# Optimization experiments

Measured on AMD Instinct MI355X. Metric: run time of the kernel, lower is better.

Reference implementation:

```python
import jax, jax.numpy as jnp
import numpy as np

N = 50000      # nodes
E = 800000     # edges (before self loops)
F_IN = 64
H = 128
OUT = 1
G = 512        # graphs in batch
NEG_SLOPE = 0.2


def setup_inputs() -> dict:
    key = jax.random.key(0)
    ks = jax.random.split(key, 16)
    s_in = 1.0 / np.sqrt(F_IN)
    s_h = 1.0 / np.sqrt(H)
    return {
        "x": jax.random.normal(ks[0], (N, F_IN), jnp.float32),
        "edge_index": jax.random.randint(ks[1], (2, E), 0, N, jnp.int64),
        "edge_weight": jax.random.uniform(ks[2], (E,), jnp.float32),
        "batch": jnp.sort(jax.random.randint(ks[3], (N,), 0, G, jnp.int64)),
        # GATv2 layer 1 (lin_l, lin_r, att, bias)
        "Wl1": jax.random.normal(ks[4], (F_IN, H), jnp.float32) * s_in,
        "bl1": jnp.zeros((H,), jnp.float32),
        "Wr1": jax.random.normal(ks[5], (F_IN, H), jnp.float32) * s_in,
        "br1": jnp.zeros((H,), jnp.float32),
        "att1": jax.random.normal(ks[6], (H,), jnp.float32) * s_h,
        "b1": jnp.zeros((H,), jnp.float32),
        # GATv2 layer 2
        "Wl2": jax.random.normal(ks[7], (H, H), jnp.float32) * s_h,
        "bl2": jnp.zeros((H,), jnp.float32),
        "Wr2": jax.random.normal(ks[8], (H, H), jnp.float32) * s_h,
        "br2": jnp.zeros((H,), jnp.float32),
        "att2": jax.random.normal(ks[9], (H,), jnp.float32) * s_h,
        "b2": jnp.zeros((H,), jnp.float32),
        # final linear head
        "Wlin": jax.random.normal(ks[10], (H, OUT), jnp.float32) * s_h,
        "blin": jnp.zeros((OUT,), jnp.float32),
    }


def gatv2_conv(x, src, dst, Wl, bl, Wr, br, att, bias):
    """PyG GATv2Conv, heads=1: alpha = softmax_dst(att . leaky_relu(xl[src]+xr[dst]));
    out[dst] = sum alpha * xl[src] + bias. Self loops already in (src, dst)."""
    xl = x @ Wl + bl                       # [N,H]  source transform
    xr = x @ Wr + br                       # [N,H]  destination transform
    e = xl[src] + xr[dst]                  # [Etot,H]
    logits = jax.nn.leaky_relu(e, NEG_SLOPE) @ att   # [Etot]
    # segment softmax over destination nodes (self loops -> every node nonempty)
    m = jax.ops.segment_max(logits, dst, num_segments=N)
    ea = jnp.exp(logits - m[dst])
    denom = jax.ops.segment_sum(ea, dst, num_segments=N)
    alpha = ea / denom[dst]
    out = jax.ops.segment_sum(alpha[:, None] * xl[src], dst, num_segments=N)
    return out + bias


def reference(x, edge_index, edge_weight, batch,
              Wl1, bl1, Wr1, br1, att1, b1,
              Wl2, bl2, Wr2, br2, att2, b2,
              Wlin, blin):
    # add self loops (GATv2Conv default add_self_loops=True); edge_weight unused by GATv2
    loops = jnp.arange(N, dtype=edge_index.dtype)
    src = jnp.concatenate([edge_index[0], loops])
    dst = jnp.concatenate([edge_index[1], loops])

    h = jax.nn.relu(gatv2_conv(x, src, dst, Wl1, bl1, Wr1, br1, att1, b1))
    h = jax.nn.relu(gatv2_conv(h, src, dst, Wl2, bl2, Wr2, br2, att2, b2))

    # global mean pool over graphs
    sums = jax.ops.segment_sum(h, batch, num_segments=G)          # [G,H]
    cnt = jax.ops.segment_sum(jnp.ones((N,), h.dtype), batch, num_segments=G)
    pooled = sums / jnp.maximum(cnt, 1.0)[:, None]

    return pooled @ Wlin + blin                                   # [G,OUT]
```

## Files before the change

### kernel.cpp

```cpp
#include <hip/hip_runtime.h>
#include <hip/hip_fp16.h>
#include <math.h>

#define N_NODES 50000
#define N_EDGES 800000
#define F_IN    64
#define H_DIM   128
#define N_GRAPH 512
#define NEG_SLOPE 0.2f

typedef __attribute__((ext_vector_type(8))) short short8;
typedef __attribute__((ext_vector_type(4))) float f32x4;
typedef __attribute__((ext_vector_type(2))) float f32x2;

#define NBIN   196
#define NBLK1  391
#define NBB    (NBIN * NBLK1)
#define SCANA_NB ((NBB + 255) / 256)

__device__ __forceinline__ void bsplit(float v, unsigned short& h, unsigned short& l) {
    unsigned u = __float_as_uint(v);
    h = (unsigned short)(u >> 16);
    float hf = __uint_as_float(u & 0xFFFF0000u);
    float r = v - hf;
    l = (unsigned short)(__float_as_uint(r) >> 16);
}
__device__ __forceinline__ float bjoin(unsigned short h, unsigned short l) {
    return __uint_as_float(((unsigned)h) << 16) + __uint_as_float(((unsigned)l) << 16);
}

#define NB_PX 3125
#define NB_PW 192
__global__ __launch_bounds__(256) void k_prep(
    const float* __restrict__ x,
    const float* __restrict__ Wl1, const float* __restrict__ Wr1,
    const float* __restrict__ Wl2, const float* __restrict__ Wr2,
    const int* __restrict__ dst,
    unsigned short* __restrict__ Xhi, unsigned short* __restrict__ Xlo,
    unsigned short* __restrict__ WThi, unsigned short* __restrict__ WTlo,
    int* __restrict__ lrank, int* __restrict__ bcnt)
{
    __shared__ int cnt_lds[NBIN];
    const int bid = blockIdx.x, tid = threadIdx.x;
    if (bid < NB_PX) {
        int i4 = (bid * 256 + tid) * 4;
        if (i4 < N_NODES * F_IN) {
            float4 v = *(const float4*)(x + i4);
            ushort4 h, l;
            bsplit(v.x, h.x, l.x); bsplit(v.y, h.y, l.y);
            bsplit(v.z, h.z, l.z); bsplit(v.w, h.w, l.w);
            *(ushort4*)(Xhi + i4) = h;
            *(ushort4*)(Xlo + i4) = l;
        }
    } else if (bid < NB_PX + NB_PW) {
        int idx = (bid - NB_PX) * 256 + tid;
        if (idx < 49152) {
            const float* W; int K, li, base, o;
            if (idx < 8192)       { W = Wl1; K = 64;  li = idx;         base = 0;     o = 0; }
            else if (idx < 16384) { W = Wr1; K = 64;  li = idx - 8192;  base = 0;     o = 1; }
            else if (idx < 32768) { W = Wl2; K = 128; li = idx - 16384; base = 16384; o = 0; }
            else                  { W = Wr2; K = 128; li = idx - 32768; base = 16384; o = 1; }
            int c = li / K, k = li - c * K;
            int g = c >> 4, n16 = c & 15;
            int kkblk = k >> 5, quad = (k >> 3) & 3, j = k & 7;
            int off = base + kkblk * 8192 + o * 4096 + g * 512 + (quad * 16 + n16) * 8 + j;
            unsigned short h, l;
            bsplit(W[k * 128 + c], h, l);
            WThi[off] = h; WTlo[off] = l;
        }
    } else {
        const int b2 = bid - NB_PX - NB_PW;
        if (tid < NBIN) cnt_lds[tid] = 0;
        __syncthreads();
#pragma unroll
        for (int it = 0; it < 8; ++it) {
            int e = b2 * 2048 + it * 256 + tid;
            if (e < N_EDGES) {
                int d = dst[e];
                lrank[e] = atomicAdd(&cnt_lds[d >> 8], 1);
            }
        }
        __syncthreads();
        if (tid < NBIN) bcnt[tid * NBLK1 + b2] = cnt_lds[tid];
    }
}

__global__ __launch_bounds__(256) void k_scanA(const int* __restrict__ bcnt,
                                               int* __restrict__ bbase,
                                               int* __restrict__ partials) {
    __shared__ int s[256];
    int t = threadIdx.x, gid = blockIdx.x * 256 + t;
    int v = (gid < NBB) ? bcnt[gid] : 0;
    s[t] = v;
    __syncthreads();
    for (int off = 1; off < 256; off <<= 1) {
        int x = (t >= off) ? s[t - off] : 0;
        __syncthreads();
        s[t] += x;
        __syncthreads();
    }
    if (gid < NBB) bbase[gid] = s[t] - v;
    if (t == 255) partials[blockIdx.x] = s[t];
}

__global__ __launch_bounds__(256) void k_scanB(int* __restrict__ bbase,
                                               const int* __restrict__ partials) {
    __shared__ int red[256];
    const int t = threadIdx.x, b = blockIdx.x;
    int acc = 0;
    for (int j = t; j < b; j += 256) acc += partials[j];
    red[t] = acc;
    __syncthreads();
    for (int off = 128; off > 0; off >>= 1) {
        if (t < off) red[t] += red[t + off];
        __syncthreads();
    }
    int base = red[0];
    int gid = b * 256 + t;
    if (gid < NBB) bbase[gid] += base;
}

__global__ __launch_bounds__(256) void k_bin2(const int* __restrict__ src,
                                              const int* __restrict__ dst,
                                              const int* __restrict__ lrank,
                                              const int* __restrict__ bbase,
                                              unsigned* __restrict__ ebin) {
    int e = blockIdx.x * 256 + threadIdx.x;
    if (e < N_EDGES) {
        int d = dst[e];
        int pos = bbase[(d >> 8) * NBLK1 + (e >> 11)] + lrank[e];
        ebin[pos] = (unsigned)src[e] | ((unsigned)(d & 255) << 16);
    }
}

__global__ __launch_bounds__(256) void k_bin3(const unsigned* __restrict__ ebin,
                                              const int* __restrict__ bbase,
                                              int* __restrict__ offsets,
                                              int* __restrict__ col_src) {
    __shared__ int cnt2[256];
    __shared__ int sc[256];
    __shared__ int cur[256];
    const int b = blockIdx.x, t = threadIdx.x;
    const int lo = bbase[b * NBLK1];
    const int hi = (b == NBIN - 1) ? N_EDGES : bbase[(b + 1) * NBLK1];

    cnt2[t] = 0;
    __syncthreads();
    for (int pos = lo + t; pos < hi; pos += 256) {
        unsigned u = ebin[pos];
        atomicAdd(&cnt2[u >> 16], 1);
    }
    __syncthreads();
    int v = cnt2[t];
    sc[t] = v;
    __syncthreads();
    for (int off = 1; off < 256; off <<= 1) {
        int x = (t >= off) ? sc[t - off] : 0;
        __syncthreads();
        sc[t] += x;
        __syncthreads();
    }
    int myoff = lo + sc[t] - v;
    int node = b * 256 + t;
    if (node < N_NODES) offsets[node] = myoff;
    cur[t] = myoff;
    if (b == NBIN - 1 && t == 0) offsets[N_NODES] = N_EDGES;
    __syncthreads();
    for (int pos = lo + t; pos < hi; pos += 256) {
        unsigned u = ebin[pos];
        int p = atomicAdd(&cur[u >> 16], 1);
        col_src[p] = (int)(u & 0xFFFFu);
    }
}

#define APITCH 40
#define GB_GEMM ((N_NODES + 63) / 64)
__global__ __launch_bounds__(256, 4) void k_gemm_mfma(
    const unsigned short* __restrict__ Xhi, const unsigned short* __restrict__ Xlo,
    const unsigned short* __restrict__ WThi, const unsigned short* __restrict__ WTlo,
    const float* __restrict__ bl, const float* __restrict__ br,
    unsigned short* __restrict__ OL, unsigned short* __restrict__ OR_, int K)
{
    __shared__ __align__(16) unsigned short Ah[64 * APITCH];
    __shared__ __align__(16) unsigned short Al[64 * APITCH];

    const int tid  = threadIdx.x;
    const int wv   = tid >> 6;
    const int lane = tid & 63;
    const int n16  = lane & 15;
    const int quad = lane >> 4;
    const int row0 = blockIdx.x * 64;

    f32x4 acc[4][2][2];
#pragma unroll
    for (int r = 0; r < 4; ++r)
#pragma unroll
        for (int c = 0; c < 2; ++c)
#pragma unroll
            for (int o = 0; o < 2; ++o) acc[r][c][o] = (f32x4)0.f;

    for (int kk = 0; kk < K; kk += 32) {
#pragma unroll
        for (int jj = 0; jj < 2; ++jj) {
            int j = tid + jj * 256;
            int part = j >> 8;
            int r = (j & 255) >> 2, sub = j & 3;
            int grow = row0 + r;
            const unsigned short* s = (part ? Xlo : Xhi) + (size_t)grow * K + kk + sub * 8;
            unsigned short* dl = (part ? Al : Ah) + r * APITCH + sub * 8;
            uint4 v = make_uint4(0u, 0u, 0u, 0u);
            if (grow < N_NODES) v = *(const uint4*)s;
            *(uint4*)dl = v;
        }
        __syncthreads();

        const unsigned short* wb_h = WThi + (size_t)(kk >> 5) * 8192;
        const unsigned short* wb_l = WTlo + (size_t)(kk >> 5) * 8192;
        short8 bh[2][2], bo[2][2];
#pragma unroll
        for (int c = 0; c < 2; ++c)
#pragma unroll
            for (int o = 0; o < 2; ++o) {
                size_t off = (size_t)o * 4096 + (size_t)(wv * 2 + c) * 512 + (size_t)lane * 8;
                bh[c][o] = *(const short8*)(wb_h + off);
                bo[c][o] = *(const short8*)(wb_l + off);
            }
#pragma unroll
        for (int r = 0; r < 4; ++r) {
            int rl = r * 16 + n16;
            short8 ah = *(const short8*)(Ah + rl * APITCH + quad * 8);
            short8 al = *(const short8*)(Al + rl * APITCH + quad * 8);
#pragma unroll
            for (int c = 0; c < 2; ++c)
#pragma unroll
                for (int o = 0; o < 2; ++o) {
                    f32x4 t = acc[r][c][o];
                    t = __builtin_amdgcn_mfma_f32_16x16x32_bf16(ah, bh[c][o], t, 0, 0, 0);
                    t = __builtin_amdgcn_mfma_f32_16x16x32_bf16(ah, bo[c][o], t, 0, 0, 0);
                    t = __builtin_amdgcn_mfma_f32_16x16x32_bf16(al, bh[c][o], t, 0, 0, 0);
                    acc[r][c][o] = t;
                }
        }
        __syncthreads();
    }

#pragma unroll
    for (int r = 0; r < 4; ++r)
#pragma unroll
        for (int c = 0; c < 2; ++c)
#pragma unroll
            for (int o = 0; o < 2; ++o) {
                int col = wv * 32 + c * 16 + n16;
                float bb = (o ? br : bl)[col];
                unsigned short* O = o ? OR_ : OL;
#pragma unroll
                for (int g = 0; g < 4; ++g) {
                    int grow = row0 + r * 16 + quad * 4 + g;
                    if (grow < N_NODES) {
                        __half hv = __float2half(acc[r][c][o][g] + bb);
                        O[(size_t)grow * 128 + col] = *(unsigned short*)&hv;
                    }
                }
            }
}

__device__ __forceinline__ float red16dpp(float v) {
    v += __int_as_float(__builtin_amdgcn_update_dpp(
             0, __float_as_int(v), 0xB1, 0xF, 0xF, true));
    v += __int_as_float(__builtin_amdgcn_update_dpp(
             0, __float_as_int(v), 0x4E, 0xF, 0xF, true));
    v += __int_as_float(__builtin_amdgcn_update_dpp(
             0, __float_as_int(v), 0x141, 0xF, 0xF, true));
    v += __int_as_float(__builtin_amdgcn_update_dpp(
             0, __float_as_int(v), 0x140, 0xF, 0xF, true));
    return v;
}

__device__ __forceinline__ void load_h8v(const unsigned short* base, size_t off,
                                         f32x2 x[4]) {
    uint4 u = *(const uint4*)(base + off);
    float2 a = __half22float2(*(__half2*)&u.x);
    float2 b = __half22float2(*(__half2*)&u.y);
    float2 c = __half22float2(*(__half2*)&u.z);
    float2 d = __half22float2(*(__half2*)&u.w);
    f32x2 v0 = {a.x, a.y}; x[0] = v0;
    f32x2 v1 = {b.x, b.y}; x[1] = v1;
    f32x2 v2 = {c.x, c.y}; x[2] = v2;
    f32x2 v3 = {d.x, d.y}; x[3] = v3;
}

__device__ __forceinline__ float dot8lk(const f32x2 x[4], const f32x2 r[4],
                                        const f32x2 a[4]) {
    f32x2 e0 = x[0] + r[0];
    f32x2 e1 = x[1] + r[1];
    f32x2 l0 = __builtin_elementwise_max(e0, NEG_SLOPE * e0);
    f32x2 l1 = __builtin_elementwise_max(e1, NEG_SLOPE * e1);
    f32x2 s0 = a[0] * l0;
    f32x2 s1 = a[1] * l1;
    f32x2 e2 = x[2] + r[2];
    f32x2 e3 = x[3] + r[3];
    f32x2 l2 = __builtin_elementwise_max(e2, NEG_SLOPE * e2);
    f32x2 l3 = __builtin_elementwise_max(e3, NEG_SLOPE * e3);
    s0 += a[2] * l2;
    s1 += a[3] * l3;
    f32x2 s = s0 + s1;
    return s.x + s.y;
}

__global__ __launch_bounds__(256) void k_edge(
    const unsigned short* __restrict__ xl, const unsigned short* __restrict__ xr,
    const float* __restrict__ att, const float* __restrict__ bias,
    const int* __restrict__ offsets, const int* __restrict__ col_src,
    unsigned short* __restrict__ outHi, unsigned short* __restrict__ outLo)
{
    int d = blockIdx.x * 4 + (threadIdx.x >> 6);
    if (d >= N_NODES) return;
    const int lane = threadIdx.x & 63;
    const int q = lane >> 4;
    const int t = lane & 15;
    const size_t dim0 = (size_t)t * 8;

    f32x2 rr[4], aa[4], xs[4];
    load_h8v(xr, (size_t)d * 128 + dim0, rr);
    {
        const float4 a0 = *(const float4*)(att + dim0);
        const float4 a1 = *(const float4*)(att + dim0 + 4);
        f32x2 w0 = {a0.x, a0.y}; aa[0] = w0;
        f32x2 w1 = {a0.z, a0.w}; aa[1] = w1;
        f32x2 w2 = {a1.x, a1.y}; aa[2] = w2;
        f32x2 w3 = {a1.z, a1.w}; aa[3] = w3;
    }
    load_h8v(xl, (size_t)d * 128 + dim0, xs);
    float sl = red16dpp(dot8lk(xs, rr, aa));

    float m = sl, thr = sl + 8.f;
    float lsum = (q == 0) ? 1.f : 0.f;
    f32x2 zero = {0.f, 0.f};
    f32x2 acc[4];
#pragma unroll
    for (int j = 0; j < 4; ++j) acc[j] = (q == 0) ? xs[j] : zero;

    const int ibeg = offsets[d], iend = offsets[d + 1];
    for (int base = ibeg; base < iend; base += 4) {
        int i = base + q;
        bool valid = (i < iend);
        int s = valid ? col_src[i] : d;
        f32x2 x[4];
        load_h8v(xl, (size_t)s * 128 + dim0, x);
        float logit = red16dpp(dot8lk(x, rr, aa));
        if (__builtin_expect(logit > thr, 0)) {
            float sc = __expf(m - logit);
            lsum *= sc;
#pragma unroll
            for (int j = 0; j < 4; ++j) acc[j] = acc[j] * sc;
            m = logit; thr = logit + 8.f;
        }
        float w = valid ? __expf(logit - m) : 0.f;
        lsum += w;
        f32x2 w2 = {w, w};
#pragma unroll
        for (int j = 0; j < 4; ++j) acc[j] += w2 * x[j];
    }

    float M = m;
    M = fmaxf(M, __shfl_xor(M, 16));
    M = fmaxf(M, __shfl_xor(M, 32));
    float sc = __expf(m - M);
    lsum *= sc;
    f32x2 sc2 = {sc, sc};
#pragma unroll
    for (int j = 0; j < 4; ++j) acc[j] = acc[j] * sc2;
#pragma unroll
    for (int off = 16; off <= 32; off <<= 1) {
        lsum += __shfl_xor(lsum, off);
#pragma unroll
        for (int j = 0; j < 4; ++j) {
            acc[j].x += __shfl_xor(acc[j].x, off);
            acc[j].y += __shfl_xor(acc[j].y, off);
        }
    }

    if (q == 0) {
        float inv = 1.f / lsum;
        const float4 b0 = *(const float4*)(bias + dim0);
        const float4 b1 = *(const float4*)(bias + dim0 + 4);
        float bv[8] = {b0.x, b0.y, b0.z, b0.w, b1.x, b1.y, b1.z, b1.w};
        float v[8];
#pragma unroll
        for (int j = 0; j < 4; ++j) {
            v[2 * j]     = fmaxf(fmaf(acc[j].x, inv, bv[2 * j]), 0.f);
            v[2 * j + 1] = fmaxf(fmaf(acc[j].y, inv, bv[2 * j + 1]), 0.f);
        }
        union { unsigned short s[8]; uint4 u; } Hh, Ll;
#pragma unroll
        for (int i2 = 0; i2 < 8; ++i2) bsplit(v[i2], Hh.s[i2], Ll.s[i2]);
        *(uint4*)(outHi + (size_t)d * 128 + dim0) = Hh.u;
        *(uint4*)(outLo + (size_t)d * 128 + dim0) = Ll.u;
    }
}

__global__ __launch_bounds__(256) void k_pool(
    const unsigned short* __restrict__ hHi, const unsigned short* __restrict__ hLo,
    const int* __restrict__ batch,
    float* __restrict__ psum, float* __restrict__ pcnt)
{
    const int tid = threadIdx.x;
    const int tx = tid & 31;
    const int ty = tid >> 5;
    const int n0 = blockIdx.x * 64;
    const int d0 = tx * 4;

    float4 acc = make_float4(0.f, 0.f, 0.f, 0.f);
    int cur = -1, crun = 0;
#pragma unroll
    for (int it = 0; it < 8; ++it) {
        int n = n0 + it * 8 + ty;
        if (n < N_NODES) {
            int g = batch[n];
            if (g != cur) {
                if (cur >= 0) {
                    atomicAdd(&psum[cur * 128 + d0 + 0], acc.x);
                    atomicAdd(&psum[cur * 128 + d0 + 1], acc.y);
                    atomicAdd(&psum[cur * 128 + d0 + 2], acc.z);
                    atomicAdd(&psum[cur * 128 + d0 + 3], acc.w);
                    if (tx == 0) atomicAdd(&pcnt[cur], (float)crun);
                }
                cur = g; acc = make_float4(0.f, 0.f, 0.f, 0.f); crun = 0;
            }
            ushort4 h = *(const ushort4*)(hHi + (size_t)n * 128 + d0);
            ushort4 l = *(const ushort4*)(hLo + (size_t)n * 128 + d0);
            acc.x += bjoin(h.x, l.x);
            acc.y += bjoin(h.y, l.y);
            acc.z += bjoin(h.z, l.z);
            acc.w += bjoin(h.w, l.w);
            crun++;
        }
    }
    if (cur >= 0) {
        atomicAdd(&psum[cur * 128 + d0 + 0], acc.x);
        atomicAdd(&psum[cur * 128 + d0 + 1], acc.y);
        atomicAdd(&psum[cur * 128 + d0 + 2], acc.z);
        atomicAdd(&psum[cur * 128 + d0 + 3], acc.w);
        if (tx == 0) atomicAdd(&pcnt[cur], (float)crun);
    }
}

__global__ __launch_bounds__(256) void k_head(
    const float* __restrict__ psum, const float* __restrict__ pcnt,
    const float* __restrict__ Wlin, const float* __restrict__ blin,
    float* __restrict__ out)
{
    int g = blockIdx.x * 4 + (threadIdx.x >> 6);
    if (g >= N_GRAPH) return;
    int lane = threadIdx.x & 63;
    float c = fmaxf(pcnt[g], 1.f);
    float2 s = *(const float2*)(psum + (size_t)g * 128 + lane * 2);
    float p = (s.x * Wlin[lane * 2] + s.y * Wlin[lane * 2 + 1]) / c;
#pragma unroll
    for (int off = 32; off > 0; off >>= 1) p += __shfl_xor(p, off);
    if (lane == 0) out[g] = p + blin[0];
}

extern "C" void kernel_launch(void* const* d_in, const int* in_sizes, int n_in,
                              void* d_out, int out_size, void* d_ws, size_t ws_size,
                              hipStream_t stream) {
    const float* x     = (const float*)d_in[0];
    const int*   ei    = (const int*)d_in[1];
    const int*   batch = (const int*)d_in[3];
    const float* Wl1 = (const float*)d_in[4],  *bl1 = (const float*)d_in[5];
    const float* Wr1 = (const float*)d_in[6],  *br1 = (const float*)d_in[7];
    const float* att1= (const float*)d_in[8],  *b1  = (const float*)d_in[9];
    const float* Wl2 = (const float*)d_in[10], *bl2 = (const float*)d_in[11];
    const float* Wr2 = (const float*)d_in[12], *br2 = (const float*)d_in[13];
    const float* att2= (const float*)d_in[14], *b2  = (const float*)d_in[15];
    const float* Wlin= (const float*)d_in[16], *blin= (const float*)d_in[17];
    float* out = (float*)d_out;

    const int* src = ei;
    const int* dst = ei + N_EDGES;

    char* p = (char*)d_ws;
    auto carve = [&](size_t bytes) {
        void* r = (void*)p;
        p += (bytes + 255) & ~(size_t)255;
        return r;
    };
    unsigned short* bufA   = (unsigned short*)carve((size_t)N_NODES * 128 * 2);
    unsigned short* bufB   = (unsigned short*)carve((size_t)N_NODES * 128 * 2);
    unsigned short* Hhi    = (unsigned short*)carve((size_t)N_NODES * 128 * 2);
    unsigned short* Hlo    = (unsigned short*)carve((size_t)N_NODES * 128 * 2);
    unsigned short* Xhi1   = (unsigned short*)carve((size_t)N_NODES * 64 * 2);
    unsigned short* Xlo1   = (unsigned short*)carve((size_t)N_NODES * 64 * 2);
    unsigned short* WThi   = (unsigned short*)carve(49152 * 2);
    unsigned short* WTlo   = (unsigned short*)carve(49152 * 2);
    int*            offsets= (int*)carve((size_t)(N_NODES + 1) * 4);
    int*            lrank  = (int*)carve((size_t)N_EDGES * 4);
    int*            bcnt   = (int*)carve((size_t)NBB * 4);
    int*            bbase  = (int*)carve((size_t)NBB * 4);
    int*            partials=(int*)carve(SCANA_NB * 4);
    unsigned*       ebin   = (unsigned*)carve((size_t)N_EDGES * 4);
    int*            col_src= (int*)carve((size_t)N_EDGES * 4);
    char* zb = (char*)carve(262144 + 2048);
    float* psum   = (float*)zb;
    float* pcnt   = (float*)(zb + 262144);
    const size_t zbytes = 262144 + 2048;

    hipMemsetAsync(zb, 0, zbytes, stream);

    k_prep<<<NB_PX + NB_PW + NBLK1, 256, 0, stream>>>(
        x, Wl1, Wr1, Wl2, Wr2, dst,
        Xhi1, Xlo1, WThi, WTlo, lrank, bcnt);

    k_gemm_mfma<<<GB_GEMM, 256, 0, stream>>>(Xhi1, Xlo1, WThi, WTlo,
                                             bl1, br1, bufA, bufB, F_IN);

    k_scanA<<<SCANA_NB, 256, 0, stream>>>(bcnt, bbase, partials);
    k_scanB<<<SCANA_NB, 256, 0, stream>>>(bbase, partials);
    k_bin2 <<<(N_EDGES + 255) / 256, 256, 0, stream>>>(src, dst, lrank, bbase, ebin);
    k_bin3 <<<NBIN, 256, 0, stream>>>(ebin, bbase, offsets, col_src);

    k_edge<<<(N_NODES + 3) / 4, 256, 0, stream>>>(
        bufA, bufB, att1, b1, offsets, col_src, Hhi, Hlo);
    k_gemm_mfma<<<GB_GEMM, 256, 0, stream>>>(Hhi, Hlo, WThi + 16384, WTlo + 16384,
                                             bl2, br2, bufA, bufB, H_DIM);
    k_edge<<<(N_NODES + 3) / 4, 256, 0, stream>>>(
        bufA, bufB, att2, b2, offsets, col_src, Hhi, Hlo);
    k_pool<<<(N_NODES + 63) / 64, 256, 0, stream>>>(Hhi, Hlo, batch, psum, pcnt);
    k_head<<<(N_GRAPH + 3) / 4, 256, 0, stream>>>(psum, pcnt, Wlin, blin, out);
}
```

Measured before the change: 286.6 us.

## Fuse x bf16 split into layer-1 GEMM and prefetch source rows in edge loop

The layer-1 GEMM now reads fp32 x directly and does the hi/lo bf16 split while staging into LDS, so k_prep no longer runs the 3125 blocks that wrote the Xhi/Xlo buffers and the GEMM no longer reads them back. The edge aggregation loop is also software-pipelined: it prefetches the next gathered xl row and the col_src index two steps ahead, hiding gather latency. The cost is more registers in k_edge and extra conversion ALU work inside the GEMM load phase.

New measurement: 270.1 us. 1.06x faster.

```diff
diff --git a/kernel.cpp b/kernel.cpp
--- a/kernel.cpp
+++ b/kernel.cpp
@@ -29,31 +29,18 @@
     return __uint_as_float(((unsigned)h) << 16) + __uint_as_float(((unsigned)l) << 16);
 }
 
-#define NB_PX 3125
 #define NB_PW 192
 __global__ __launch_bounds__(256) void k_prep(
-    const float* __restrict__ x,
     const float* __restrict__ Wl1, const float* __restrict__ Wr1,
     const float* __restrict__ Wl2, const float* __restrict__ Wr2,
     const int* __restrict__ dst,
-    unsigned short* __restrict__ Xhi, unsigned short* __restrict__ Xlo,
     unsigned short* __restrict__ WThi, unsigned short* __restrict__ WTlo,
     int* __restrict__ lrank, int* __restrict__ bcnt)
 {
     __shared__ int cnt_lds[NBIN];
     const int bid = blockIdx.x, tid = threadIdx.x;
-    if (bid < NB_PX) {
-        int i4 = (bid * 256 + tid) * 4;
-        if (i4 < N_NODES * F_IN) {
-            float4 v = *(const float4*)(x + i4);
-            ushort4 h, l;
-            bsplit(v.x, h.x, l.x); bsplit(v.y, h.y, l.y);
-            bsplit(v.z, h.z, l.z); bsplit(v.w, h.w, l.w);
-            *(ushort4*)(Xhi + i4) = h;
-            *(ushort4*)(Xlo + i4) = l;
-        }
-    } else if (bid < NB_PX + NB_PW) {
-        int idx = (bid - NB_PX) * 256 + tid;
+    if (bid < NB_PW) {
+        int idx = bid * 256 + tid;
         if (idx < 49152) {
             const float* W; int K, li, base, o;
             if (idx < 8192)       { W = Wl1; K = 64;  li = idx;         base = 0;     o = 0; }
@@ -69,7 +56,7 @@
             WThi[off] = h; WTlo[off] = l;
         }
     } else {
-        const int b2 = bid - NB_PX - NB_PW;
+        const int b2 = bid - NB_PW;
         if (tid < NBIN) cnt_lds[tid] = 0;
         __syncthreads();
 #pragma unroll
@@ -175,21 +162,23 @@
 
 #define APITCH 40
 #define GB_GEMM ((N_NODES + 63) / 64)
-__global__ __launch_bounds__(256, 4) void k_gemm_mfma(
+
+template <bool F32SRC>
+__device__ __forceinline__ void gemm_body(
+    unsigned short* __restrict__ Ah, unsigned short* __restrict__ Al,
+    const float* __restrict__ Xf,
     const unsigned short* __restrict__ Xhi, const unsigned short* __restrict__ Xlo,
     const unsigned short* __restrict__ WThi, const unsigned short* __restrict__ WTlo,
     const float* __restrict__ bl, const float* __restrict__ br,
-    unsigned short* __restrict__ OL, unsigned short* __restrict__ OR_, int K)
-{
-    __shared__ __align__(16) unsigned short Ah[64 * APITCH];
-    __shared__ __align__(16) unsigned short Al[64 * APITCH];
-
+    unsigned short* __restrict__ OL, unsigned short* __restrict__ OR_,
+    int K, int blk)
+{
     const int tid  = threadIdx.x;
     const int wv   = tid >> 6;
     const int lane = tid & 63;
     const int n16  = lane & 15;
     const int quad = lane >> 4;
-    const int row0 = blockIdx.x * 64;
+    const int row0 = blk * 64;
 
     f32x4 acc[4][2][2];
 #pragma unroll
@@ -200,17 +189,36 @@
             for (int o = 0; o < 2; ++o) acc[r][c][o] = (f32x4)0.f;
 
     for (int kk = 0; kk < K; kk += 32) {
-#pragma unroll
-        for (int jj = 0; jj < 2; ++jj) {
-            int j = tid + jj * 256;
-            int part = j >> 8;
-            int r = (j & 255) >> 2, sub = j & 3;
+        if (F32SRC) {
+            int r = tid >> 2, sub = tid & 3;
             int grow = row0 + r;
-            const unsigned short* s = (part ? Xlo : Xhi) + (size_t)grow * K + kk + sub * 8;
-            unsigned short* dl = (part ? Al : Ah) + r * APITCH + sub * 8;
-            uint4 v = make_uint4(0u, 0u, 0u, 0u);
-            if (grow < N_NODES) v = *(const uint4*)s;
-            *(uint4*)dl = v;
+            float4 v0 = make_float4(0.f, 0.f, 0.f, 0.f);
+            float4 v1 = make_float4(0.f, 0.f, 0.f, 0.f);
+            if (grow < N_NODES) {
+                const float* s = Xf + (size_t)grow * K + kk + sub * 8;
+                v0 = *(const float4*)s;
+                v1 = *(const float4*)(s + 4);
+            }
+            union { unsigned short s[8]; uint4 u; } Hh, Ll;
+            bsplit(v0.x, Hh.s[0], Ll.s[0]); bsplit(v0.y, Hh.s[1], Ll.s[1]);
+            bsplit(v0.z, Hh.s[2], Ll.s[2]); bsplit(v0.w, Hh.s[3], Ll.s[3]);
+            bsplit(v1.x, Hh.s[4], Ll.s[4]); bsplit(v1.y, Hh.s[5], Ll.s[5]);
+            bsplit(v1.z, Hh.s[6], Ll.s[6]); bsplit(v1.w, Hh.s[7], Ll.s[7]);
+            *(uint4*)(Ah + r * APITCH + sub * 8) = Hh.u;
+            *(uint4*)(Al + r * APITCH + sub * 8) = Ll.u;
+        } else {
+#pragma unroll
+            for (int jj = 0; jj < 2; ++jj) {
+                int j = tid + jj * 256;
+                int part = j >> 8;
+                int r = (j & 255) >> 2, sub = j & 3;
+                int grow = row0 + r;
+                const unsigned short* s = (part ? Xlo : Xhi) + (size_t)grow * K + kk + sub * 8;
+                unsigned short* dl = (part ? Al : Ah) + r * APITCH + sub * 8;
+                uint4 v = make_uint4(0u, 0u, 0u, 0u);
+                if (grow < N_NODES) v = *(const uint4*)s;
+                *(uint4*)dl = v;
+            }
         }
         __syncthreads();
 
@@ -262,6 +270,28 @@
                     }
                 }
             }
+}
+
+__global__ __launch_bounds__(256, 4) void k_gemm_f32(
+    const float* __restrict__ Xf,
+    const unsigned short* __restrict__ WThi, const unsigned short* __restrict__ WTlo,
+    const float* __restrict__ bl, const float* __restrict__ br,
+    unsigned short* __restrict__ OL, unsigned short* __restrict__ OR_, int K)
+{
+    __shared__ __align__(16) unsigned short Ah[64 * APITCH];
+    __shared__ __align__(16) unsigned short Al[64 * APITCH];
+    gemm_body<true>(Ah, Al, Xf, nullptr, nullptr, WThi, WTlo, bl, br, OL, OR_, K, blockIdx.x);
+}
+
+__global__ __launch_bounds__(256, 4) void k_gemm_mfma(
+    const unsigned short* __restrict__ Xhi, const unsigned short* __restrict__ Xlo,
+    const unsigned short* __restrict__ WThi, const unsigned short* __restrict__ WTlo,
+    const float* __restrict__ bl, const float* __restrict__ br,
+    unsigned short* __restrict__ OL, unsigned short* __restrict__ OR_, int K)
+{
+    __shared__ __align__(16) unsigned short Ah[64 * APITCH];
+    __shared__ __align__(16) unsigned short Al[64 * APITCH];
+    gemm_body<false>(Ah, Al, nullptr, Xhi, Xlo, WThi, WTlo, bl, br, OL, OR_, K, blockIdx.x);
 }
 
 __device__ __forceinline__ float red16dpp(float v) {
@@ -276,9 +306,7 @@
     return v;
 }
 
-__device__ __forceinline__ void load_h8v(const unsigned short* base, size_t off,
-                                         f32x2 x[4]) {
-    uint4 u = *(const uint4*)(base + off);
+__device__ __forceinline__ void cvt_h8(uint4 u, f32x2 x[4]) {
     float2 a = __half22float2(*(__half2*)&u.x);
     float2 b = __half22float2(*(__half2*)&u.y);
     float2 c = __half22float2(*(__half2*)&u.z);
@@ -287,6 +315,11 @@
     f32x2 v1 = {b.x, b.y}; x[1] = v1;
     f32x2 v2 = {c.x, c.y}; x[2] = v2;
     f32x2 v3 = {d.x, d.y}; x[3] = v3;
+}
+__device__ __forceinline__ void load_h8v(const unsigned short* base, size_t off,
+                                         f32x2 x[4]) {
+    uint4 u = *(const uint4*)(base + off);
+    cvt_h8(u, x);
 }
 
 __device__ __forceinline__ float dot8lk(const f32x2 x[4], const f32x2 r[4],
@@ -341,12 +374,22 @@
     for (int j = 0; j < 4; ++j) acc[j] = (q == 0) ? xs[j] : zero;
 
     const int ibeg = offsets[d], iend = offsets[d + 1];
+    int ia = ibeg + q;
+    bool vA = ia < iend;
+    int sA = vA ? col_src[ia] : d;
+    uint4 uA = *(const uint4*)(xl + (size_t)sA * 128 + dim0);
+    int ib = ia + 4;
+    bool vB = ib < iend;
+    int sB = vB ? col_src[ib] : d;
+
     for (int base = ibeg; base < iend; base += 4) {
-        int i = base + q;
-        bool valid = (i < iend);
-        int s = valid ? col_src[i] : d;
+        uint4 uB = *(const uint4*)(xl + (size_t)sB * 128 + dim0);
+        int ic = base + 8 + q;
+        bool vC = ic < iend;
+        int sC = vC ? col_src[ic] : d;
+
         f32x2 x[4];
-        load_h8v(xl, (size_t)s * 128 + dim0, x);
+        cvt_h8(uA, x);
         float logit = red16dpp(dot8lk(x, rr, aa));
         if (__builtin_expect(logit > thr, 0)) {
             float sc = __expf(m - logit);
@@ -355,11 +398,13 @@
             for (int j = 0; j < 4; ++j) acc[j] = acc[j] * sc;
             m = logit; thr = logit + 8.f;
         }
-        float w = valid ? __expf(logit - m) : 0.f;
+        float w = vA ? __expf(logit - m) : 0.f;
         lsum += w;
         f32x2 w2 = {w, w};
 #pragma unroll
         for (int j = 0; j < 4; ++j) acc[j] += w2 * x[j];
+
+        uA = uB; vA = vB; sB = sC; vB = vC;
     }
 
     float M = m;
@@ -489,8 +534,6 @@
     unsigned short* bufB   = (unsigned short*)carve((size_t)N_NODES * 128 * 2);
     unsigned short* Hhi    = (unsigned short*)carve((size_t)N_NODES * 128 * 2);
     unsigned short* Hlo    = (unsigned short*)carve((size_t)N_NODES * 128 * 2);
-    unsigned short* Xhi1   = (unsigned short*)carve((size_t)N_NODES * 64 * 2);
-    unsigned short* Xlo1   = (unsigned short*)carve((size_t)N_NODES * 64 * 2);
     unsigned short* WThi   = (unsigned short*)carve(49152 * 2);
     unsigned short* WTlo   = (unsigned short*)carve(49152 * 2);
     int*            offsets= (int*)carve((size_t)(N_NODES + 1) * 4);
@@ -507,12 +550,11 @@
 
     hipMemsetAsync(zb, 0, zbytes, stream);
 
-    k_prep<<<NB_PX + NB_PW + NBLK1, 256, 0, stream>>>(
-        x, Wl1, Wr1, Wl2, Wr2, dst,
-        Xhi1, Xlo1, WThi, WTlo, lrank, bcnt);
-
-    k_gemm_mfma<<<GB_GEMM, 256, 0, stream>>>(Xhi1, Xlo1, WThi, WTlo,
-                                             bl1, br1, bufA, bufB, F_IN);
+    k_prep<<<NB_PW + NBLK1, 256, 0, stream>>>(
+        Wl1, Wr1, Wl2, Wr2, dst, WThi, WTlo, lrank, bcnt);
+
+    k_gemm_f32<<<GB_GEMM, 256, 0, stream>>>(x, WThi, WTlo,
+                                            bl1, br1, bufA, bufB, F_IN);
 
     k_scanA<<<SCANA_NB, 256, 0, stream>>>(bcnt, bbase, partials);
     k_scanB<<<SCANA_NB, 256, 0, stream>>>(bbase, partials);
```
